# Optimization experiments

Hardware: AMD Instinct MI355X
Metric: run time of the kernel (lower is better)

Reference implementation:

```python
import jax, jax.numpy as jnp
import numpy as np

N_RNA, N_PROT = 50000, 20000
S, E = 4, 500000
D_IN = 1024


def setup_inputs() -> dict:
    key = jax.random.key(0)
    ks = jax.random.split(key, 12)
    return {
        "rna_rows": jax.random.randint(ks[0], (S, E), 0, N_RNA, dtype=jnp.int32),
        "rna_cols": jax.random.randint(ks[1], (S, E), 0, N_PROT, dtype=jnp.int32),
        "rna_vals": jax.random.uniform(ks[2], (S, E), dtype=jnp.float32),
        "prot_rows": jax.random.randint(ks[3], (S, E), 0, N_PROT, dtype=jnp.int32),
        "prot_cols": jax.random.randint(ks[4], (S, E), 0, N_RNA, dtype=jnp.int32),
        "prot_vals": jax.random.uniform(ks[5], (S, E), dtype=jnp.float32),
        "H_rna": jax.random.normal(ks[6], (N_RNA, D_IN), dtype=jnp.float32),
        "H_prot": jax.random.normal(ks[7], (N_PROT, D_IN), dtype=jnp.float32),
        "w0": jax.random.normal(ks[8], (S, 1024, 128), dtype=jnp.float32) * 0.04,
        "sw0": jax.random.normal(ks[9], (1024, 512), dtype=jnp.float32) * 0.04,
        "w1": jax.random.normal(ks[10], (S, 512, 64), dtype=jnp.float32) * 0.06,
        "sw1": jax.random.normal(ks[11], (512, 256), dtype=jnp.float32) * 0.06,
    }


def _spmm_all(rows, cols, vals, x, n_out):
    # rows/cols/vals: [S, E]; x: [S, n_in, k] -> [S, n_out, k]
    def one(r, c, v, xs):
        return jax.ops.segment_sum(v[:, None] * xs[c], r, num_segments=n_out)
    return jax.vmap(one)(rows, cols, vals, x)


def reference(rna_rows, rna_cols, rna_vals, prot_rows, prot_cols, prot_vals,
              H_rna, H_prot, w0, sw0, w1, sw1):
    n_rna, n_prot = H_rna.shape[0], H_prot.shape[0]
    for W, SW in ((w0, sw0), (w1, sw1)):
        s, _, k = W.shape
        # per-relation dense transform: [S, n, k]
        tmp_u = jnp.einsum('nd,sdk->snk', H_rna, W)
        tmp_v = jnp.einsum('nd,sdk->snk', H_prot, W)
        # sparse aggregation across the bipartite graph
        rna_h = _spmm_all(rna_rows, rna_cols, rna_vals, tmp_v, n_rna)     # [S, n_rna, k]
        prot_h = _spmm_all(prot_rows, prot_cols, prot_vals, tmp_u, n_prot)
        # concat over relations (matches torch.cat along dim=1)
        rna_h = jnp.transpose(rna_h, (1, 0, 2)).reshape(n_rna, s * k)
        prot_h = jnp.transpose(prot_h, (1, 0, 2)).reshape(n_prot, s * k)
        # self-loop residual; dropout=0.0 (eval) is identity; relu activation
        H_rna = jax.nn.relu(rna_h + H_rna @ SW)
        H_prot = jax.nn.relu(prot_h + H_prot @ SW)
    return H_rna, H_prot
```

## Files before the change

### kernel.cpp

```cpp
#include <hip/hip_runtime.h>
#include <hip/hip_bf16.h>


typedef unsigned short u16;
typedef short s16x8 __attribute__((ext_vector_type(8)));
typedef float f32x4 __attribute__((ext_vector_type(4)));
typedef __attribute__((ext_vector_type(8))) unsigned short u16x8;
typedef __attribute__((ext_vector_type(2))) unsigned short u16x2;

__device__ __forceinline__ u16 f2bf(float x) {
    unsigned u = __float_as_uint(x);
    return (u16)((u + 0x7fff + ((u >> 16) & 1)) >> 16);
}
__device__ __forceinline__ float bf2f(u16 h) {
    return __uint_as_float(((unsigned)h) << 16);
}

__device__ __forceinline__ void gload16(const u16* g, u16* l) {
    __builtin_amdgcn_global_load_lds(
        (const __attribute__((address_space(1))) unsigned int*)g,
        (__attribute__((address_space(3))) unsigned int*)l,
        16, 0, 0);
}

__global__ __launch_bounds__(256)
void gemm_bf16_kernel(const u16* __restrict__ Ah, const u16* __restrict__ Bh,
                      u16* __restrict__ T16, int ldt,
                      float* __restrict__ Yb, int ldb, int tmpw,
                      int K, int nxmask, int nxshift)
{
    __shared__ u16 lds[2][2][4096];

    const int nwg = gridDim.x;
    const int q   = nwg >> 3, r8 = nwg & 7;
    const int xcd = blockIdx.x & 7, pos = blockIdx.x >> 3;
    const int lin = (xcd < r8 ? xcd * (q + 1) : r8 * (q + 1) + (xcd - r8) * q) + pos;
    const int bm0 = (lin >> nxshift) * 128;
    const int bn0 = (lin & nxmask) * 128;

    const int tid  = threadIdx.x;
    const int lane = tid & 63;
    const int wid  = tid >> 6;
    const int wr   = wid >> 1;
    const int wc   = wid & 1;

    const int srow = tid >> 2;
    const int scol = ((tid & 3) ^ ((tid >> 3) & 3)) * 8;
    const size_t aoff0 = (size_t)(bm0 + srow) * K + scol;
    const size_t aoff1 = (size_t)(bm0 + srow + 64) * K + scol;
    const size_t boff0 = (size_t)(bn0 + srow) * K + scol;
    const size_t boff1 = (size_t)(bn0 + srow + 64) * K + scol;
    const int c0 = tid * 8;
    const int c1 = 2048 + tid * 8;

    u16* L0 = &lds[0][0][0];

    f32x4 zero = {0.f, 0.f, 0.f, 0.f};
    f32x4 acc[4][4];
    #pragma unroll
    for (int i = 0; i < 4; ++i)
        #pragma unroll
        for (int j = 0; j < 4; ++j) acc[i][j] = zero;

    const int fchunk = (((lane >> 4) ^ ((lane >> 1) & 3))) * 8;
    const int a_fr = (wr * 64 + (lane & 15)) * 32 + fchunk;
    const int b_fr = (wc * 64 + (lane & 15)) * 32 + fchunk;

    const int nk = K >> 5;

    {
        u16* L = L0;
        gload16(Ah + aoff0, L + c0);          gload16(Ah + aoff1, L + c1);
        gload16(Bh + boff0, L + 4096 + c0);   gload16(Bh + boff1, L + 4096 + c1);
    }
    int cur = 0;
    for (int t = 0; t < nk; ++t) {
        if (t + 1 < nk) {
            const int k0 = (t + 1) * 32;
            u16* L = L0 + (cur ^ 1) * 8192;
            gload16(Ah + aoff0 + k0, L + c0);         gload16(Ah + aoff1 + k0, L + c1);
            gload16(Bh + boff0 + k0, L + 4096 + c0);  gload16(Bh + boff1 + k0, L + 4096 + c1);
            asm volatile("s_waitcnt vmcnt(4)\n\ts_barrier" ::: "memory");
        } else {
            asm volatile("s_waitcnt vmcnt(0)\n\ts_barrier" ::: "memory");
        }
        const u16* L = L0 + cur * 8192;
        s16x8 bh[4];
        #pragma unroll
        for (int nf = 0; nf < 4; ++nf)
            bh[nf] = *(const s16x8*)(L + 4096 + b_fr + nf * 512);
        #pragma unroll
        for (int mf = 0; mf < 4; ++mf) {
            s16x8 ahv = *(const s16x8*)(L + a_fr + mf * 512);
            #pragma unroll
            for (int nf = 0; nf < 4; ++nf)
                acc[mf][nf] = __builtin_amdgcn_mfma_f32_16x16x32_bf16(ahv, bh[nf], acc[mf][nf], 0, 0, 0);
        }
        asm volatile("s_barrier" ::: "memory");
        cur ^= 1;
    }

    if (bn0 < tmpw) {
        #pragma unroll
        for (int mf = 0; mf < 4; ++mf) {
            const int row0 = bm0 + wr * 64 + mf * 16 + (lane >> 4) * 4;
            #pragma unroll
            for (int nf = 0; nf < 4; ++nf) {
                const int col = bn0 + wc * 64 + nf * 16 + (lane & 15);
                #pragma unroll
                for (int r = 0; r < 4; ++r)
                    T16[(size_t)(row0 + r) * ldt + col] = f2bf(acc[mf][nf][r]);
            }
        }
    } else {
        #pragma unroll
        for (int mf = 0; mf < 4; ++mf) {
            const int row0 = bm0 + wr * 64 + mf * 16 + (lane >> 4) * 4;
            #pragma unroll
            for (int nf = 0; nf < 4; ++nf) {
                const int col = bn0 + wc * 64 + nf * 16 + (lane & 15) - tmpw;
                #pragma unroll
                for (int r = 0; r < 4; ++r)
                    Yb[(size_t)(row0 + r) * ldb + col] = acc[mf][nf][r];
            }
        }
    }
}

__global__ __launch_bounds__(256)
void cvt_bf16_kernel(const float* __restrict__ A, u16* __restrict__ Hh,
                     int M, int kshift)
{
    const size_t g  = (size_t)blockIdx.x * 256 + threadIdx.x;
    const size_t i8 = g * 8;
    const int row   = (int)(i8 >> kshift);
    f32x4 a = {0.f, 0.f, 0.f, 0.f}, b = {0.f, 0.f, 0.f, 0.f};
    if (row < M) {
        a = *(const f32x4*)(A + i8);
        b = *(const f32x4*)(A + i8 + 4);
    }
    u16x8 h;
    #pragma unroll
    for (int j = 0; j < 4; ++j) { h[j] = f2bf(a[j]); h[4 + j] = f2bf(b[j]); }
    *(u16x8*)(Hh + i8) = h;
}

__global__ __launch_bounds__(256)
void zero_u16_kernel(u16* __restrict__ a, int n)
{
    int i = blockIdx.x * 256 + threadIdx.x;
    if (i < n) a[i] = 0;
}

__global__ __launch_bounds__(256)
void zero2_i32_kernel(int* __restrict__ a, int na, int* __restrict__ b, int nb)
{
    int i = blockIdx.x * 256 + threadIdx.x;
    if (i < na) a[i] = 0;
    if (i < nb) b[i] = 0;
}

__global__ __launch_bounds__(256)
void hist2_kernel(const int* __restrict__ rowsR, const int* __restrict__ rowsP,
                  int* __restrict__ cntR, int* __restrict__ cntP,
                  int NR, int NP, int E)
{
    int s = blockIdx.y;
    int e = blockIdx.x * 256 + threadIdx.x;
    if (e >= E) return;
    if (blockIdx.z == 0) atomicAdd(cntR + s * NR + rowsR[(size_t)s * E + e], 1);
    else                 atomicAdd(cntP + s * NP + rowsP[(size_t)s * E + e], 1);
}

__global__ __launch_bounds__(256)
void scan_block2_kernel(const int* __restrict__ cR, int* __restrict__ rpR,
                        int* __restrict__ bsR, int NR, int np1R, int NBR,
                        const int* __restrict__ cP, int* __restrict__ rpP,
                        int* __restrict__ bsP, int NP, int np1P, int NBP)
{
    const int side = blockIdx.z;
    const int NB = side ? NBP : NBR;
    if ((int)blockIdx.x >= NB) return;
    const int N = side ? NP : NR;
    const int np1 = side ? np1P : np1R;
    const int* counts = side ? cP : cR;
    int* rowptr = side ? rpP : rpR;
    int* blocksum = side ? bsP : bsR;

    __shared__ int sd[256];
    int s = blockIdx.y;
    int i = blockIdx.x * 256 + threadIdx.x;
    int tid = threadIdx.x;
    int v = (i < N) ? counts[s * N + i] : 0;
    sd[tid] = v;
    __syncthreads();
    #pragma unroll
    for (int off = 1; off < 256; off <<= 1) {
        int t = (tid >= off) ? sd[tid - off] : 0;
        __syncthreads();
        sd[tid] += t;
        __syncthreads();
    }
    if (i < N) rowptr[s * np1 + i] = sd[tid] - v;
    if (tid == 255) blocksum[s * NB + blockIdx.x] = sd[255];
}

__global__ __launch_bounds__(256)
void scan_aux2_kernel(int* __restrict__ bsR, int NBR, int* __restrict__ bsP, int NBP)
{
    const int side = blockIdx.x >> 2;
    const int s = blockIdx.x & 3;
    int* blocksum = side ? bsP : bsR;
    const int NB = side ? NBP : NBR;

    __shared__ int sd[256];
    int tid = threadIdx.x;
    int v = (tid < NB) ? blocksum[s * NB + tid] : 0;
    sd[tid] = v;
    __syncthreads();
    #pragma unroll
    for (int off = 1; off < 256; off <<= 1) {
        int t = (tid >= off) ? sd[tid - off] : 0;
        __syncthreads();
        sd[tid] += t;
        __syncthreads();
    }
    if (tid < NB) blocksum[s * NB + tid] = sd[tid] - v;
}

__global__ __launch_bounds__(256)
void finalize2_kernel(int* __restrict__ rpR, const int* __restrict__ bsR,
                      int* __restrict__ curR, int NR, int np1R, int NBR,
                      int* __restrict__ rpP, const int* __restrict__ bsP,
                      int* __restrict__ curP, int NP, int np1P, int NBP, int E)
{
    const int side = blockIdx.z;
    const int NB = side ? NBP : NBR;
    if ((int)blockIdx.x >= NB) return;
    const int N = side ? NP : NR;
    const int np1 = side ? np1P : np1R;
    int* rowptr = side ? rpP : rpR;
    const int* blocksum = side ? bsP : bsR;
    int* cursor = side ? curP : curR;

    int s = blockIdx.y;
    int i = blockIdx.x * 256 + threadIdx.x;
    if (i < N) {
        int v = rowptr[s * np1 + i] + blocksum[s * NB + blockIdx.x];
        rowptr[s * np1 + i] = v;
        cursor[s * N + i] = v;
    }
    if (i == N) rowptr[s * np1 + N] = E;
}

__global__ __launch_bounds__(256)
void fill_sliced_kernel(const int* __restrict__ rowsR, const int* __restrict__ colsR,
                        const float* __restrict__ valsR,
                        const int* __restrict__ rowsP, const int* __restrict__ colsP,
                        const float* __restrict__ valsP,
                        int* __restrict__ curR, int* __restrict__ curP,
                        int2* __restrict__ evR, int2* __restrict__ evP,
                        int NR, int NP, int E)
{
    const int slice = blockIdx.x & 7;
    const int chunk = blockIdx.x >> 3;
    const int s     = blockIdx.y;
    const int side  = blockIdx.z;
    const int N          = side ? NP : NR;
    const int* rows      = side ? rowsP : rowsR;
    const int* cols      = side ? colsP : colsR;
    const float* vals    = side ? valsP : valsR;
    int* cursor          = side ? curP : curR;
    int2* ev             = side ? evP : evR;

    const int Nsl = (N + 7) >> 3;
    const int r0 = slice * Nsl;
    const int r1 = min(N, r0 + Nsl);

    const int e0 = chunk * 1024 + threadIdx.x * 4;
    if (e0 >= E) return;
    const size_t base = (size_t)s * E;

    if (e0 + 4 <= E) {
        int4   r4 = *(const int4*)(rows + base + e0);
        int4   c4 = *(const int4*)(cols + base + e0);
        float4 v4 = *(const float4*)(vals + base + e0);
        int   rr[4] = {r4.x, r4.y, r4.z, r4.w};
        int   cc[4] = {c4.x, c4.y, c4.z, c4.w};
        float vv[4] = {v4.x, v4.y, v4.z, v4.w};
        #pragma unroll
        for (int j = 0; j < 4; ++j) {
            if (rr[j] >= r0 && rr[j] < r1) {
                int pos = atomicAdd(cursor + s * N + rr[j], 1);
                ev[base + pos] = make_int2(cc[j], __float_as_int(vv[j]));
            }
        }
    } else {
        for (int j = 0; j < 4 && e0 + j < E; ++j) {
            int r = rows[base + e0 + j];
            if (r >= r0 && r < r1) {
                int pos = atomicAdd(cursor + s * N + r, 1);
                ev[base + pos] = make_int2(cols[base + e0 + j],
                                           __float_as_int(vals[base + e0 + j]));
            }
        }
    }
}

template<int KCH, int MODE>
__global__ __launch_bounds__(256)
void spmm2_kernel(const int* __restrict__ rpR, const int* __restrict__ rpP,
                  int np1R, int np1P,
                  const int2* __restrict__ evRg, const int2* __restrict__ evPg,
                  const u16* __restrict__ InR, const u16* __restrict__ InP, int ldi,
                  float* __restrict__ BaseR, float* __restrict__ BaseP, int ldb,
                  u16* __restrict__ OHR, u16* __restrict__ OHP,
                  float* __restrict__ OFR, float* __restrict__ OFP, int ldo,
                  int NR, int E)
{
    int r = blockIdx.x;
    const int s    = threadIdx.x >> 6;
    const int lane = threadIdx.x & 63;
    const int* rp; const int2* ev; const u16* In; float* Base; int np1;
    u16* OH; float* OF;
    if (r < NR) { rp = rpR; ev = evRg; In = InR; Base = BaseR; np1 = np1R;
                  OH = OHR; OF = OFR; }
    else { r -= NR; rp = rpP; ev = evPg; In = InP; Base = BaseP; np1 = np1P;
           OH = OHP; OF = OFP; }
    int e0 = __builtin_amdgcn_readfirstlane(rp[s * np1 + r]);
    int e1 = __builtin_amdgcn_readfirstlane(rp[s * np1 + r + 1]);
    if (MODE == 0 && e0 == e1) return;
    ev += (size_t)s * E;

    if (KCH == 128) {
        const int col = s * 128 + lane * 2;
        float ax = 0.f, ay = 0.f;
        int e = e0;
        for (; e + 3 < e1; e += 4) {
            int2 pa = ev[e], pb = ev[e+1], pc = ev[e+2], pd = ev[e+3];
            float va = __int_as_float(pa.y), vb = __int_as_float(pb.y);
            float vc = __int_as_float(pc.y), vd = __int_as_float(pd.y);
            u16x2 xa = *(const u16x2*)(In + (size_t)pa.x * ldi + col);
            u16x2 xb = *(const u16x2*)(In + (size_t)pb.x * ldi + col);
            u16x2 xc = *(const u16x2*)(In + (size_t)pc.x * ldi + col);
            u16x2 xd = *(const u16x2*)(In + (size_t)pd.x * ldi + col);
            ax += va * bf2f(xa[0]) + vb * bf2f(xb[0]) + vc * bf2f(xc[0]) + vd * bf2f(xd[0]);
            ay += va * bf2f(xa[1]) + vb * bf2f(xb[1]) + vc * bf2f(xc[1]) + vd * bf2f(xd[1]);
        }
        for (; e < e1; ++e) {
            int2 p = ev[e];
            float v = __int_as_float(p.y);
            u16x2 x = *(const u16x2*)(In + (size_t)p.x * ldi + col);
            ax += v * bf2f(x[0]);  ay += v * bf2f(x[1]);
        }
        if (MODE == 0) {
            float2* o = (float2*)(Base + (size_t)r * ldb + col);
            float2 cv = *o; cv.x += ax; cv.y += ay; *o = cv;
        } else if (MODE == 1) {
            const float2 b = *(const float2*)(Base + (size_t)r * ldb + col);
            float fx = fmaxf(b.x + ax, 0.f), fy = fmaxf(b.y + ay, 0.f);
            u16x2 h = {f2bf(fx), f2bf(fy)};
            *(u16x2*)(OH + (size_t)r * ldo + col) = h;
        } else {
            const float2 b = *(const float2*)(Base + (size_t)r * ldb + col);
            float2 o; o.x = fmaxf(b.x + ax, 0.f); o.y = fmaxf(b.y + ay, 0.f);
            *(float2*)(OF + (size_t)r * ldo + col) = o;
        }
    } else {
        const int col = s * 64 + lane;
        float acc = 0.f;
        int e = e0;
        for (; e + 3 < e1; e += 4) {
            int2 pa = ev[e], pb = ev[e+1], pc = ev[e+2], pd = ev[e+3];
            acc += __int_as_float(pa.y) * bf2f(In[(size_t)pa.x * ldi + col])
                 + __int_as_float(pb.y) * bf2f(In[(size_t)pb.x * ldi + col])
                 + __int_as_float(pc.y) * bf2f(In[(size_t)pc.x * ldi + col])
                 + __int_as_float(pd.y) * bf2f(In[(size_t)pd.x * ldi + col]);
        }
        for (; e < e1; ++e) {
            int2 p = ev[e];
            acc += __int_as_float(p.y) * bf2f(In[(size_t)p.x * ldi + col]);
        }
        if (MODE == 0) {
            Base[(size_t)r * ldb + col] += acc;
        } else {
            OF[(size_t)r * ldo + col] = fmaxf(Base[(size_t)r * ldb + col] + acc, 0.f);
        }
    }
}

__global__ __launch_bounds__(256)
void relu_out_kernel(const float* __restrict__ Z, float* __restrict__ out, int M)
{
    int g = blockIdx.x * 256 + threadIdx.x;
    if (g >= M * 256) return;
    out[g] = fmaxf(Z[g], 0.f);
}

__global__ __launch_bounds__(256)
void pack_b0_kernel(const float* __restrict__ w0, const float* __restrict__ sw0,
                    u16* __restrict__ Bh)
{
    int g = blockIdx.x * 256 + threadIdx.x;
    int j = g >> 10, d = g & 1023;
    float v;
    if (j < 512) v = w0[((size_t)(j >> 7) * 1024 + d) * 128 + (j & 127)];
    else         v = sw0[(size_t)d * 512 + (j - 512)];
    Bh[g] = f2bf(v);
}

__global__ __launch_bounds__(256)
void pack_b1_kernel(const float* __restrict__ w1, const float* __restrict__ sw1,
                    u16* __restrict__ Bh)
{
    int g = blockIdx.x * 256 + threadIdx.x;
    int j = g >> 9, d = g & 511;
    float v;
    if (j < 256) v = w1[((size_t)(j >> 6) * 512 + d) * 64 + (j & 63)];
    else         v = sw1[(size_t)d * 256 + (j - 256)];
    Bh[g] = f2bf(v);
}

extern "C" void kernel_launch(void* const* d_in, const int* in_sizes, int n_in,
                              void* d_out, int out_size, void* d_ws, size_t ws_size,
                              hipStream_t stream)
{
    const int*   rna_rows  = (const int*)  d_in[0];
    const int*   rna_cols  = (const int*)  d_in[1];
    const float* rna_vals  = (const float*)d_in[2];
    const int*   prot_rows = (const int*)  d_in[3];
    const int*   prot_cols = (const int*)  d_in[4];
    const float* prot_vals = (const float*)d_in[5];
    const float* H_rna     = (const float*)d_in[6];
    const float* H_prot    = (const float*)d_in[7];
    const float* w0        = (const float*)d_in[8];
    const float* sw0       = (const float*)d_in[9];
    const float* w1        = (const float*)d_in[10];
    const float* sw1       = (const float*)d_in[11];

    const int NRNA = 50000, NPROT = 20000, S = 4, E = 500000;
    const int MP_RNA = 50048, MP_PROT = 20096;
    const int MP_ALL = MP_RNA + MP_PROT;
    const int NP1_R = NRNA + 1, NP1_P = NPROT + 1;
    const int NB_R = (NRNA + 255) / 256;
    const int NB_P = (NPROT + 255) / 256;
    const int EB   = (E + 255) / 256;
    const int EB4  = (E + 1023) / 1024;

    char* ws = (char*)d_ws;
    size_t off = 0;
    float* Ybase = (float*)(ws + off); off += (size_t)MP_ALL * 512 * 4;
    u16*   Tmp0  = (u16*)  (ws + off); off += (size_t)MP_ALL * 512 * 2;
    u16*   Ahbig = (u16*)  (ws + off); off += (size_t)MP_ALL * 1024 * 2;
    u16*   B0h   = (u16*)  (ws + off); off += (size_t)1024 * 1024 * 2;
    u16*   B1h   = (u16*)  (ws + off); off += (size_t)512 * 512 * 2;
    size_t base_bytes = off;

    u16* AhR = Ahbig;
    u16* AhP = Ahbig + (size_t)MP_RNA * 512;

    size_t csr_bytes = 0;
    csr_bytes += (size_t)S * E * 8 * 2;
    csr_bytes += ((size_t)S * (NRNA * 2 + NP1_R + NB_R)) * 4;
    csr_bytes += ((size_t)S * (NPROT * 2 + NP1_P + NB_P)) * 4;
    const bool csr_in_ws = (ws_size >= base_bytes + csr_bytes);

    char* csr = csr_in_ws ? (ws + base_bytes) : (char*)d_out;
    size_t coff = 0;
    int2*  evR     = (int2*) (csr + coff); coff += (size_t)S * E * 8;
    int2*  evP     = (int2*) (csr + coff); coff += (size_t)S * E * 8;
    int*   countsR = (int*)  (csr + coff); coff += (size_t)S * NRNA * 4;
    int*   rowptrR = (int*)  (csr + coff); coff += (size_t)S * NP1_R * 4;
    int*   cursorR = (int*)  (csr + coff); coff += (size_t)S * NRNA * 4;
    int*   bsumR   = (int*)  (csr + coff); coff += (size_t)S * NB_R * 4;
    int*   countsP = (int*)  (csr + coff); coff += (size_t)S * NPROT * 4;
    int*   rowptrP = (int*)  (csr + coff); coff += (size_t)S * NP1_P * 4;
    int*   cursorP = (int*)  (csr + coff); coff += (size_t)S * NPROT * 4;
    int*   bsumP   = (int*)  (csr + coff); coff += (size_t)S * NB_P * 4;

    dim3 blk(256);
    float* out = (float*)d_out;

    pack_b0_kernel<<<(1024 * 1024) / 256, blk, 0, stream>>>(w0, sw0, B0h);
    pack_b1_kernel<<<(512 * 512) / 256, blk, 0, stream>>>(w1, sw1, B1h);

    zero2_i32_kernel<<<(S * NRNA + 255) / 256, blk, 0, stream>>>(countsR, S * NRNA,
                                                                 countsP, S * NPROT);
    hist2_kernel<<<dim3(EB, S, 2), blk, 0, stream>>>(rna_rows, prot_rows,
                                                     countsR, countsP, NRNA, NPROT, E);
    scan_block2_kernel<<<dim3(NB_R, S, 2), blk, 0, stream>>>(
        countsR, rowptrR, bsumR, NRNA, NP1_R, NB_R,
        countsP, rowptrP, bsumP, NPROT, NP1_P, NB_P);
    scan_aux2_kernel<<<8, blk, 0, stream>>>(bsumR, NB_R, bsumP, NB_P);
    finalize2_kernel<<<dim3(NB_R, S, 2), blk, 0, stream>>>(
        rowptrR, bsumR, cursorR, NRNA, NP1_R, NB_R,
        rowptrP, bsumP, cursorP, NPROT, NP1_P, NB_P, E);
    fill_sliced_kernel<<<dim3(EB4 * 8, S, 2), blk, 0, stream>>>(
        rna_rows, rna_cols, rna_vals, prot_rows, prot_cols, prot_vals,
        cursorR, cursorP, evR, evP, NRNA, NPROT, E);

    cvt_bf16_kernel<<<MP_RNA / 2, blk, 0, stream>>>(H_rna, Ahbig, NRNA, 10);
    cvt_bf16_kernel<<<MP_PROT / 2, blk, 0, stream>>>(H_prot, Ahbig + (size_t)MP_RNA * 1024,
                                                     NPROT, 10);
    gemm_bf16_kernel<<<8 * (MP_ALL / 128), blk, 0, stream>>>(
        Ahbig, B0h, Tmp0, 512, Ybase, 512, 512, 1024, 7, 3);

    spmm2_kernel<128, 1><<<NRNA + NPROT, blk, 0, stream>>>(
        rowptrR, rowptrP, NP1_R, NP1_P, evR, evP,
        Tmp0 + (size_t)MP_RNA * 512,
        Tmp0,
        512,
        Ybase, Ybase + (size_t)MP_RNA * 512, 512,
        AhR, AhP, nullptr, nullptr, 512,
        NRNA, E);

    zero_u16_kernel<<<(48 * 512 + 255) / 256, blk, 0, stream>>>(
        AhR + (size_t)NRNA * 512, 48 * 512);
    zero_u16_kernel<<<(96 * 512 + 255) / 256, blk, 0, stream>>>(
        AhP + (size_t)NPROT * 512, 96 * 512);

    gemm_bf16_kernel<<<4 * (MP_ALL / 128), blk, 0, stream>>>(
        Ahbig, B1h, Tmp0, 256, Ybase, 256, 256, 512, 3, 2);

    if (csr_in_ws) {
        spmm2_kernel<64, 2><<<NRNA + NPROT, blk, 0, stream>>>(
            rowptrR, rowptrP, NP1_R, NP1_P, evR, evP,
            Tmp0 + (size_t)MP_RNA * 256, Tmp0, 256,
            Ybase, Ybase + (size_t)MP_RNA * 256, 256,
            nullptr, nullptr,
            out, out + (size_t)NRNA * 256, 256,
            NRNA, E);
    } else {
        spmm2_kernel<64, 0><<<NRNA + NPROT, blk, 0, stream>>>(
            rowptrR, rowptrP, NP1_R, NP1_P, evR, evP,
            Tmp0 + (size_t)MP_RNA * 256, Tmp0, 256,
            Ybase, Ybase + (size_t)MP_RNA * 256, 256,
            nullptr, nullptr,
            nullptr, nullptr, 0,
            NRNA, E);
        relu_out_kernel<<<(NRNA * 256) / 256, blk, 0, stream>>>(Ybase, out, NRNA);
        relu_out_kernel<<<(NPROT * 256) / 256, blk, 0, stream>>>(
            Ybase + (size_t)MP_RNA * 256, out + (size_t)NRNA * 256, NPROT);
    }
}
```

Measured before the change: 1.157 ms.

## Store GEMM self-loop residual in bf16 alongside transform output to cut traffic

The GEMM epilogue now writes every output column as bf16 into one interleaved buffer, replacing the separate fp32 residual buffer. The SpMM kernels read the residual as bf16, and the fill kernel now loads cols/vals only for edges in its row slice. This is meant to halve residual write and read bandwidth and simplify the epilogue, at the cost of rounding the self-loop term to bf16 and wider strided rows.

```diff
diff --git a/kernel.cpp b/kernel.cpp
--- a/kernel.cpp
+++ b/kernel.cpp
@@ -25,8 +25,7 @@
 
 __global__ __launch_bounds__(256)
 void gemm_bf16_kernel(const u16* __restrict__ Ah, const u16* __restrict__ Bh,
-                      u16* __restrict__ T16, int ldt,
-                      float* __restrict__ Yb, int ldb, int tmpw,
+                      u16* __restrict__ Y, int ldy,
                       int K, int nxmask, int nxshift)
 {
     __shared__ u16 lds[2][2][4096];
@@ -100,29 +99,15 @@
         cur ^= 1;
     }
 
-    if (bn0 < tmpw) {
+    #pragma unroll
+    for (int mf = 0; mf < 4; ++mf) {
+        const int row0 = bm0 + wr * 64 + mf * 16 + (lane >> 4) * 4;
         #pragma unroll
-        for (int mf = 0; mf < 4; ++mf) {
-            const int row0 = bm0 + wr * 64 + mf * 16 + (lane >> 4) * 4;
+        for (int nf = 0; nf < 4; ++nf) {
+            const int col = bn0 + wc * 64 + nf * 16 + (lane & 15);
             #pragma unroll
-            for (int nf = 0; nf < 4; ++nf) {
-                const int col = bn0 + wc * 64 + nf * 16 + (lane & 15);
-                #pragma unroll
-                for (int r = 0; r < 4; ++r)
-                    T16[(size_t)(row0 + r) * ldt + col] = f2bf(acc[mf][nf][r]);
-            }
-        }
-    } else {
-        #pragma unroll
-        for (int mf = 0; mf < 4; ++mf) {
-            const int row0 = bm0 + wr * 64 + mf * 16 + (lane >> 4) * 4;
-            #pragma unroll
-            for (int nf = 0; nf < 4; ++nf) {
-                const int col = bn0 + wc * 64 + nf * 16 + (lane & 15) - tmpw;
-                #pragma unroll
-                for (int r = 0; r < 4; ++r)
-                    Yb[(size_t)(row0 + r) * ldb + col] = acc[mf][nf][r];
-            }
+            for (int r = 0; r < 4; ++r)
+                Y[(size_t)(row0 + r) * ldy + col] = f2bf(acc[mf][nf][r]);
         }
     }
 }
@@ -282,17 +267,14 @@
     const size_t base = (size_t)s * E;
 
     if (e0 + 4 <= E) {
-        int4   r4 = *(const int4*)(rows + base + e0);
-        int4   c4 = *(const int4*)(cols + base + e0);
-        float4 v4 = *(const float4*)(vals + base + e0);
-        int   rr[4] = {r4.x, r4.y, r4.z, r4.w};
-        int   cc[4] = {c4.x, c4.y, c4.z, c4.w};
-        float vv[4] = {v4.x, v4.y, v4.z, v4.w};
+        int4 r4 = *(const int4*)(rows + base + e0);
+        int rr[4] = {r4.x, r4.y, r4.z, r4.w};
         #pragma unroll
         for (int j = 0; j < 4; ++j) {
             if (rr[j] >= r0 && rr[j] < r1) {
                 int pos = atomicAdd(cursor + s * N + rr[j], 1);
-                ev[base + pos] = make_int2(cc[j], __float_as_int(vv[j]));
+                ev[base + pos] = make_int2(cols[base + e0 + j],
+                                           __float_as_int(vals[base + e0 + j]));
             }
         }
     } else {
@@ -313,7 +295,7 @@
                   int np1R, int np1P,
                   const int2* __restrict__ evRg, const int2* __restrict__ evPg,
                   const u16* __restrict__ InR, const u16* __restrict__ InP, int ldi,
-                  float* __restrict__ BaseR, float* __restrict__ BaseP, int ldb,
+                  u16* __restrict__ BaseR, u16* __restrict__ BaseP, int ldb,
                   u16* __restrict__ OHR, u16* __restrict__ OHP,
                   float* __restrict__ OFR, float* __restrict__ OFP, int ldo,
                   int NR, int E)
@@ -321,7 +303,7 @@
     int r = blockIdx.x;
     const int s    = threadIdx.x >> 6;
     const int lane = threadIdx.x & 63;
-    const int* rp; const int2* ev; const u16* In; float* Base; int np1;
+    const int* rp; const int2* ev; const u16* In; u16* Base; int np1;
     u16* OH; float* OF;
     if (r < NR) { rp = rpR; ev = evRg; In = InR; Base = BaseR; np1 = np1R;
                   OH = OHR; OF = OFR; }
@@ -353,17 +335,19 @@
             u16x2 x = *(const u16x2*)(In + (size_t)p.x * ldi + col);
             ax += v * bf2f(x[0]);  ay += v * bf2f(x[1]);
         }
+        u16x2* bp = (u16x2*)(Base + (size_t)r * ldb + col);
+        u16x2 b = *bp;
         if (MODE == 0) {
-            float2* o = (float2*)(Base + (size_t)r * ldb + col);
-            float2 cv = *o; cv.x += ax; cv.y += ay; *o = cv;
+            u16x2 nb = {f2bf(bf2f(b[0]) + ax), f2bf(bf2f(b[1]) + ay)};
+            *bp = nb;
         } else if (MODE == 1) {
-            const float2 b = *(const float2*)(Base + (size_t)r * ldb + col);
-            float fx = fmaxf(b.x + ax, 0.f), fy = fmaxf(b.y + ay, 0.f);
-            u16x2 h = {f2bf(fx), f2bf(fy)};
+            u16x2 h = {f2bf(fmaxf(bf2f(b[0]) + ax, 0.f)),
+                       f2bf(fmaxf(bf2f(b[1]) + ay, 0.f))};
             *(u16x2*)(OH + (size_t)r * ldo + col) = h;
         } else {
-            const float2 b = *(const float2*)(Base + (size_t)r * ldb + col);
-            float2 o; o.x = fmaxf(b.x + ax, 0.f); o.y = fmaxf(b.y + ay, 0.f);
+            float2 o;
+            o.x = fmaxf(bf2f(b[0]) + ax, 0.f);
+            o.y = fmaxf(bf2f(b[1]) + ay, 0.f);
             *(float2*)(OF + (size_t)r * ldo + col) = o;
         }
     } else {
@@ -381,20 +365,24 @@
             int2 p = ev[e];
             acc += __int_as_float(p.y) * bf2f(In[(size_t)p.x * ldi + col]);
         }
+        u16* bp = Base + (size_t)r * ldb + col;
         if (MODE == 0) {
-            Base[(size_t)r * ldb + col] += acc;
+            *bp = f2bf(bf2f(*bp) + acc);
         } else {
-            OF[(size_t)r * ldo + col] = fmaxf(Base[(size_t)r * ldb + col] + acc, 0.f);
-        }
-    }
-}
-
-__global__ __launch_bounds__(256)
-void relu_out_kernel(const float* __restrict__ Z, float* __restrict__ out, int M)
+            OF[(size_t)r * ldo + col] = fmaxf(bf2f(*bp) + acc, 0.f);
+        }
+    }
+}
+
+__global__ __launch_bounds__(256)
+void relu_out_kernel(const u16* __restrict__ Z, int ld, int coff,
+                     float* __restrict__ out, int M)
 {
     int g = blockIdx.x * 256 + threadIdx.x;
     if (g >= M * 256) return;
-    out[g] = fmaxf(Z[g], 0.f);
+    int row = g >> 8;
+    int col = g & 255;
+    out[g] = fmaxf(bf2f(Z[(size_t)row * ld + coff + col]), 0.f);
 }
 
 __global__ __launch_bounds__(256)
@@ -449,8 +437,7 @@
 
     char* ws = (char*)d_ws;
     size_t off = 0;
-    float* Ybase = (float*)(ws + off); off += (size_t)MP_ALL * 512 * 4;
-    u16*   Tmp0  = (u16*)  (ws + off); off += (size_t)MP_ALL * 512 * 2;
+    u16*   Y16   = (u16*)  (ws + off); off += (size_t)MP_ALL * 1024 * 2;
     u16*   Ahbig = (u16*)  (ws + off); off += (size_t)MP_ALL * 1024 * 2;
     u16*   B0h   = (u16*)  (ws + off); off += (size_t)1024 * 1024 * 2;
     u16*   B1h   = (u16*)  (ws + off); off += (size_t)512 * 512 * 2;
@@ -503,14 +490,14 @@
     cvt_bf16_kernel<<<MP_PROT / 2, blk, 0, stream>>>(H_prot, Ahbig + (size_t)MP_RNA * 1024,
                                                      NPROT, 10);
     gemm_bf16_kernel<<<8 * (MP_ALL / 128), blk, 0, stream>>>(
-        Ahbig, B0h, Tmp0, 512, Ybase, 512, 512, 1024, 7, 3);
+        Ahbig, B0h, Y16, 1024, 1024, 7, 3);
 
     spmm2_kernel<128, 1><<<NRNA + NPROT, blk, 0, stream>>>(
         rowptrR, rowptrP, NP1_R, NP1_P, evR, evP,
-        Tmp0 + (size_t)MP_RNA * 512,
-        Tmp0,
-        512,
-        Ybase, Ybase + (size_t)MP_RNA * 512, 512,
+        Y16 + (size_t)MP_RNA * 1024,
+        Y16,
+        1024,
+        Y16 + 512, Y16 + (size_t)MP_RNA * 1024 + 512, 1024,
         AhR, AhP, nullptr, nullptr, 512,
         NRNA, E);
 
@@ -520,26 +507,26 @@
         AhP + (size_t)NPROT * 512, 96 * 512);
 
     gemm_bf16_kernel<<<4 * (MP_ALL / 128), blk, 0, stream>>>(
-        Ahbig, B1h, Tmp0, 256, Ybase, 256, 256, 512, 3, 2);
+        Ahbig, B1h, Y16, 512, 512, 3, 2);
 
     if (csr_in_ws) {
         spmm2_kernel<64, 2><<<NRNA + NPROT, blk, 0, stream>>>(
             rowptrR, rowptrP, NP1_R, NP1_P, evR, evP,
-            Tmp0 + (size_t)MP_RNA * 256, Tmp0, 256,
-            Ybase, Ybase + (size_t)MP_RNA * 256, 256,
+            Y16 + (size_t)MP_RNA * 512, Y16, 512,
+            Y16 + 256, Y16 + (size_t)MP_RNA * 512 + 256, 512,
             nullptr, nullptr,
             out, out + (size_t)NRNA * 256, 256,
             NRNA, E);
     } else {
         spmm2_kernel<64, 0><<<NRNA + NPROT, blk, 0, stream>>>(
             rowptrR, rowptrP, NP1_R, NP1_P, evR, evP,
-            Tmp0 + (size_t)MP_RNA * 256, Tmp0, 256,
-            Ybase, Ybase + (size_t)MP_RNA * 256, 256,
+            Y16 + (size_t)MP_RNA * 512, Y16, 512,
+            Y16 + 256, Y16 + (size_t)MP_RNA * 512 + 256, 512,
             nullptr, nullptr,
             nullptr, nullptr, 0,
             NRNA, E);
-        relu_out_kernel<<<(NRNA * 256) / 256, blk, 0, stream>>>(Ybase, out, NRNA);
+        relu_out_kernel<<<(NRNA * 256) / 256, blk, 0, stream>>>(Y16, 512, 256, out, NRNA);
         relu_out_kernel<<<(NPROT * 256) / 256, blk, 0, stream>>>(
-            Ybase + (size_t)MP_RNA * 256, out + (size_t)NRNA * 256, NPROT);
-    }
-}
+            Y16 + (size_t)MP_RNA * 512, 512, 256, out + (size_t)NRNA * 256, NPROT);
+    }
+}
```

After: 1.103 ms. -4.7%, faster.
